# Optimization experiments

Measured on AMD Instinct MI355X. Metric: run time of the kernel, lower is better.

## Reference

```python
import jax, jax.numpy as jnp
import numpy as np

K = 32768          # random Fourier features of the integrand
MAX_DEPTH = 4      # fixed unroll depth of the adaptive quadtree


def _f_eval(px, py, w, ax, ay, phi):
    # integrand f(x,y) = sum_k w_k * cos(ax_k x + ay_k y + phi_k)
    theta = px[..., None] * ax + py[..., None] * ay + phi  # (..., K)
    return jnp.cos(theta) @ w


def _simpson_cells(xl, xr, yl, yr, w, ax, ay, phi):
    # 2D Simpson estimate per cell; matches _quad_simpsons2D_mem (center point
    # fp[4] has coefficient 0 in the original formula, so it is skipped).
    mx = (xl + xr) * 0.5
    my = (yl + yr) * 0.5
    px = jnp.stack([xl, mx, xr, xl, xr, xl, mx, xr], axis=-1)  # (N, 8)
    py = jnp.stack([yl, yl, yl, my, my, yr, yr, yr], axis=-1)
    fv = _f_eval(px, py, w, ax, ay, phi)                        # (N, 8)
    hx = jnp.abs(xr - xl)
    hy = jnp.abs(yr - yl)
    return hx * hy / 12.0 * (
        -(fv[..., 0] + fv[..., 2] + fv[..., 5] + fv[..., 7])
        + 4.0 * (fv[..., 1] + fv[..., 3] + fv[..., 4] + fv[..., 6]))


def _split(xl, xr, yl, yr):
    # children in quadrant order q0 (LL), q1 (LR), q2 (UL), q3 (UR), interleaved
    mx = (xl + xr) * 0.5
    my = (yl + yr) * 0.5
    cxl = jnp.stack([xl, mx, xl, mx], -1).reshape(-1)
    cxr = jnp.stack([mx, xr, mx, xr], -1).reshape(-1)
    cyl = jnp.stack([yl, yl, my, my], -1).reshape(-1)
    cyr = jnp.stack([my, my, yr, yr], -1).reshape(-1)
    return cxl, cxr, cyl, cyr


def _adaptive_simpson2d(xa, xb, ya, yb, eps, w, ax, ay, phi):
    xl = jnp.reshape(xa, (1,)); xr = jnp.reshape(xb, (1,))
    yl = jnp.reshape(ya, (1,)); yr = jnp.reshape(yb, (1,))
    bounds = [(xl, xr, yl, yr)]
    S = [_simpson_cells(xl, xr, yl, yr, w, ax, ay, phi)]  # (4**d,) per depth
    wholes = [S[0]]  # 'whole' passed into the asr call for each cell
    for d in range(1, MAX_DEPTH + 1):
        b = _split(*bounds[d - 1])
        bounds.append(b)
        Sd = _simpson_cells(*b, w, ax, ay, phi)
        S.append(Sd)
        W = Sd.reshape(-1, 4)
        # NOTE: original code passes q0 (not q3) as 'whole' for quadrant 3 --
        # this bug is reproduced faithfully.
        wholes.append(jnp.stack([W[:, 0], W[:, 1], W[:, 2], W[:, 0]], -1).reshape(-1))
    val = None
    for d in range(MAX_DEPTH - 1, -1, -1):
        sum_q = S[d + 1].reshape(-1, 4).sum(-1)
        delta = sum_q - wholes[d]
        corrected = sum_q + delta / 15.0
        if d == MAX_DEPTH - 1:
            val = corrected  # truncate recursion at max depth
        else:
            child_sum = val.reshape(-1, 4).sum(-1)
            eps_d = eps / (4.0 ** d)  # eps is quartered at each recursion level
            val = jnp.where(jnp.abs(delta) <= 15.0 * eps_d, corrected, child_sum)
    return val[0]


def setup_inputs() -> dict:
    key = jax.random.key(0)
    k1, k2, k3, k4 = jax.random.split(key, 4)
    w = jax.random.normal(k1, (K,), jnp.float32) / np.float32(np.sqrt(K))
    ax = jax.random.normal(k2, (K,), jnp.float32) * 6.0
    ay = jax.random.normal(k3, (K,), jnp.float32) * 6.0
    phi = jax.random.uniform(k4, (K,), jnp.float32) * np.float32(2.0 * np.pi)
    return {"xa": jnp.float32(0.0), "xb": jnp.float32(1.0),
            "ya": jnp.float32(0.0), "yb": jnp.float32(1.0),
            "eps": jnp.float32(1e-6),
            "w": w, "ax": ax, "ay": ay, "phi": phi}


def reference(xa, xb, ya, yb, eps, w, ax, ay, phi):
    return _adaptive_simpson2d(xa, xb, ya, yb, eps, w, ax, ay, phi)
```

## Files before the change

kernel.cpp:

```cpp
#include <hip/hip_runtime.h>
#include <math.h>

#define KFEAT 32768
#define GRID_N 33
#define NPTS (GRID_N * GRID_N)
#define NQ 833
#define QSTRIDE 836
#define QGROUPS (QSTRIDE / 4)
#define PTS_PER_BLOCK 8
#define PBLOCKS ((NQ + PTS_PER_BLOCK - 1) / PTS_PER_BLOCK)
#define SPLITK 8
#define KG 4

#define INV2PI 0.15915494309189535f

__device__ __forceinline__ void q_to_grid(int q, int& gx, int& gy) {
  int rp = q / 50;
  int rem = q - 50 * rp;
  if (rem < 33) { gy = 2 * rp;     gx = rem; }
  else          { gy = 2 * rp + 1; gx = (rem - 33) * 2; }
}

__device__ __forceinline__ float cos_rev(float rev) {
  float fr, c;
  asm("v_fract_f32 %0, %1" : "=v"(fr) : "v"(rev));
  asm("v_cos_f32 %0, %1" : "=v"(c) : "v"(fr));
  return c;
}

__global__ __launch_bounds__(256) void eval_grid_kernel(
    const float4* __restrict__ w4, const float4* __restrict__ ax4,
    const float4* __restrict__ ay4, const float4* __restrict__ phi4,
    const float* __restrict__ xa_p, const float* __restrict__ xb_p,
    const float* __restrict__ ya_p, const float* __restrict__ yb_p,
    float* __restrict__ Fpart) {
  const int tid = threadIdx.x;
  const int pblk = blockIdx.x;
  const int split = blockIdx.y;
  const float xa = xa_p[0], xb = xb_p[0];
  const float ya = ya_p[0], yb = yb_p[0];
  const float sx = (xb - xa) * (1.0f / 32.0f);
  const float sy = (yb - ya) * (1.0f / 32.0f);

  const int p0 = pblk * PTS_PER_BLOCK;
  float x[PTS_PER_BLOCK], y[PTS_PER_BLOCK];
#pragma unroll
  for (int j = 0; j < PTS_PER_BLOCK; ++j) {
    int q = min(p0 + j, NQ - 1);
    int gx, gy;
    q_to_grid(q, gx, gy);
    x[j] = fmaf((float)gx, sx, xa);
    y[j] = fmaf((float)gy, sy, ya);
  }

  const int base4 = split * ((KFEAT / 4) / SPLITK);
  float4 A[KG], B[KG], P[KG], W[KG];
#pragma unroll
  for (int u = 0; u < KG; ++u) {
    const int idx = base4 + tid + 256 * u;
    A[u] = ax4[idx];
    B[u] = ay4[idx];
    P[u] = phi4[idx];
    W[u] = w4[idx];
  }
#pragma unroll
  for (int u = 0; u < KG; ++u) {
    A[u].x *= INV2PI; A[u].y *= INV2PI; A[u].z *= INV2PI; A[u].w *= INV2PI;
    B[u].x *= INV2PI; B[u].y *= INV2PI; B[u].z *= INV2PI; B[u].w *= INV2PI;
    P[u].x *= INV2PI; P[u].y *= INV2PI; P[u].z *= INV2PI; P[u].w *= INV2PI;
  }

  float acc[PTS_PER_BLOCK];
#pragma unroll
  for (int j = 0; j < PTS_PER_BLOCK; ++j) acc[j] = 0.0f;

#pragma unroll
  for (int u = 0; u < KG; ++u) {
#pragma unroll
    for (int j = 0; j < PTS_PER_BLOCK; ++j) {
      float r0 = fmaf(A[u].x, x[j], fmaf(B[u].x, y[j], P[u].x));
      float r1 = fmaf(A[u].y, x[j], fmaf(B[u].y, y[j], P[u].y));
      float r2 = fmaf(A[u].z, x[j], fmaf(B[u].z, y[j], P[u].z));
      float r3 = fmaf(A[u].w, x[j], fmaf(B[u].w, y[j], P[u].w));
      float s = fmaf(W[u].x, cos_rev(r0), fmaf(W[u].y, cos_rev(r1),
                fmaf(W[u].z, cos_rev(r2), W[u].w * cos_rev(r3))));
      acc[j] += s;
    }
  }

  __shared__ float red[4][PTS_PER_BLOCK];
#pragma unroll
  for (int j = 0; j < PTS_PER_BLOCK; ++j) {
    float v = acc[j];
#pragma unroll
    for (int off = 32; off > 0; off >>= 1) v += __shfl_down(v, off, 64);
    if ((tid & 63) == 0) red[tid >> 6][j] = v;
  }
  __syncthreads();
  if (tid < PTS_PER_BLOCK) {
    const int j = tid;
    float v = red[0][j] + red[1][j] + red[2][j] + red[3][j];
    int q = p0 + j;
    if (q < NQ) Fpart[split * QSTRIDE + q] = v;
  }
}

__device__ __forceinline__ int compact_bits(int v, int shift) {
  int r = (v >> shift) & 1;
  r |= ((v >> (shift + 2)) & 1) << 1;
  r |= ((v >> (shift + 4)) & 1) << 2;
  r |= ((v >> (shift + 6)) & 1) << 3;
  return r;
}

__device__ __forceinline__ float simpson_cell(const float* __restrict__ F,
                                              int d, int cell, float hx,
                                              float hy) {
  const int ix = compact_bits(cell, 0);
  const int iy = compact_bits(cell, 1);
  const int s = 5 - d;
  const int h = 1 << (s - 1);
  const int gx0 = ix << s, gx1 = gx0 + h, gx2 = gx0 + 2 * h;
  const int gy0 = iy << s, gy1 = gy0 + h, gy2 = gy0 + 2 * h;
  const float f0 = F[gy0 * GRID_N + gx0];
  const float f1 = F[gy0 * GRID_N + gx1];
  const float f2 = F[gy0 * GRID_N + gx2];
  const float f3 = F[gy1 * GRID_N + gx0];
  const float f4 = F[gy1 * GRID_N + gx2];
  const float f5 = F[gy2 * GRID_N + gx0];
  const float f6 = F[gy2 * GRID_N + gx1];
  const float f7 = F[gy2 * GRID_N + gx2];
  return hx * hy * (1.0f / 12.0f) *
         (-(f0 + f2 + f5 + f7) + 4.0f * (f1 + f3 + f4 + f6));
}

__global__ __launch_bounds__(1024) void combine_kernel(
    const float* __restrict__ Fpart, const float* __restrict__ xa_p,
    const float* __restrict__ xb_p, const float* __restrict__ ya_p,
    const float* __restrict__ yb_p, const float* __restrict__ eps_p,
    float* __restrict__ out) {
  __shared__ alignas(16) float Fq[2][QSTRIDE];
  __shared__ float Fs[NPTS];
  __shared__ float S4[256], S3[64], S2[16], S1[4], S0[1];
  __shared__ float val3[64], val2[16], val1[4];
  const int t = threadIdx.x;
  const float xa = *xa_p, xb = *xb_p, ya = *ya_p, yb = *yb_p, eps = *eps_p;
  const float HX = fabsf(xb - xa), HY = fabsf(yb - ya);

  if (t < 2 * QGROUPS) {
    const int quad = (t >= QGROUPS) ? 1 : 0;
    const int g = t - quad * QGROUPS;
    const float4* Fp4 = (const float4*)Fpart;
    float4 s = make_float4(0.0f, 0.0f, 0.0f, 0.0f);
#pragma unroll
    for (int sp = 0; sp < 4; ++sp) {
      float4 v = Fp4[(quad * 4 + sp) * QGROUPS + g];
      s.x += v.x; s.y += v.y; s.z += v.z; s.w += v.w;
    }
    ((float4*)&Fq[quad][0])[g] = s;
  }
  __syncthreads();

  if (t < NQ) {
    float v = Fq[0][t] + Fq[1][t];
    int gx, gy;
    int rp = t / 50;
    int rem = t - 50 * rp;
    if (rem < 33) { gy = 2 * rp;     gx = rem; }
    else          { gy = 2 * rp + 1; gx = (rem - 33) * 2; }
    Fs[gy * GRID_N + gx] = v;
  }
  __syncthreads();

  if (t < 256) {
    S4[t] = simpson_cell(Fs, 4, t, HX * 0.0625f, HY * 0.0625f);
    if (t < 64) {
      S3[t] = simpson_cell(Fs, 3, t, HX * 0.125f, HY * 0.125f);
    } else if (t < 80) {
      S2[t - 64] = simpson_cell(Fs, 2, t - 64, HX * 0.25f, HY * 0.25f);
    } else if (t < 84) {
      S1[t - 80] = simpson_cell(Fs, 1, t - 80, HX * 0.5f, HY * 0.5f);
    } else if (t == 84) {
      S0[0] = simpson_cell(Fs, 0, 0, HX, HY);
    }
  }
  __syncthreads();

  if (t < 64) {
    float sumq = ((S4[4 * t] + S4[4 * t + 1]) + S4[4 * t + 2]) + S4[4 * t + 3];
    float whole = ((t & 3) == 3) ? S3[t & ~3] : S3[t];
    float delta = sumq - whole;
    val3[t] = sumq + delta * (1.0f / 15.0f);
  }
  __syncthreads();

  if (t < 16) {
    float sumq = ((S3[4 * t] + S3[4 * t + 1]) + S3[4 * t + 2]) + S3[4 * t + 3];
    float whole = ((t & 3) == 3) ? S2[t & ~3] : S2[t];
    float delta = sumq - whole;
    float corrected = sumq + delta * (1.0f / 15.0f);
    float child =
        ((val3[4 * t] + val3[4 * t + 1]) + val3[4 * t + 2]) + val3[4 * t + 3];
    float eps_d = eps * (1.0f / 16.0f);
    val2[t] = (fabsf(delta) <= 15.0f * eps_d) ? corrected : child;
  }
  __syncthreads();

  if (t < 4) {
    float sumq = ((S2[4 * t] + S2[4 * t + 1]) + S2[4 * t + 2]) + S2[4 * t + 3];
    float whole = ((t & 3) == 3) ? S1[t & ~3] : S1[t];
    float delta = sumq - whole;
    float corrected = sumq + delta * (1.0f / 15.0f);
    float child =
        ((val2[4 * t] + val2[4 * t + 1]) + val2[4 * t + 2]) + val2[4 * t + 3];
    float eps_d = eps * 0.25f;
    val1[t] = (fabsf(delta) <= 15.0f * eps_d) ? corrected : child;
  }
  __syncthreads();

  if (t == 0) {
    float sumq = ((S1[0] + S1[1]) + S1[2]) + S1[3];
    float delta = sumq - S0[0];
    float corrected = sumq + delta * (1.0f / 15.0f);
    float child = ((val1[0] + val1[1]) + val1[2]) + val1[3];
    out[0] = (fabsf(delta) <= 15.0f * eps) ? corrected : child;
  }
}

extern "C" void kernel_launch(void* const* d_in, const int* in_sizes, int n_in,
                              void* d_out, int out_size, void* d_ws,
                              size_t ws_size, hipStream_t stream) {
  const float* xa = (const float*)d_in[0];
  const float* xb = (const float*)d_in[1];
  const float* ya = (const float*)d_in[2];
  const float* yb = (const float*)d_in[3];
  const float* eps = (const float*)d_in[4];
  const float4* w4 = (const float4*)d_in[5];
  const float4* ax4 = (const float4*)d_in[6];
  const float4* ay4 = (const float4*)d_in[7];
  const float4* phi4 = (const float4*)d_in[8];
  float* out = (float*)d_out;
  float* Fpart = (float*)d_ws;

  dim3 grid(PBLOCKS, SPLITK);
  eval_grid_kernel<<<grid, 256, 0, stream>>>(w4, ax4, ay4, phi4, xa, xb, ya,
                                             yb, Fpart);
  combine_kernel<<<1, 1024, 0, stream>>>(Fpart, xa, xb, ya, yb, eps, out);
}
```

Baseline: 17.35 us.

## Evaluate grid rows with Chebyshev cosine recurrence instead of per-point cos

Each block now handles one row pair of the grid and, per feature, computes cosines along a row with the three-term recurrence cos((n+1)b+a) = 2cos(b)cos(nb+a) - cos((n-1)b+a). Only a few hardware cos calls are needed per feature per row, replacing one transcendental per point. The split over K grows to 32 with fewer blocks along the points, and the combine kernel is changed to reduce 32 partials using 256 threads. The recurrence can accumulate rounding error over 33 steps, and 50 accumulators per thread raise register pressure.

```diff
diff --git a/kernel.cpp b/kernel.cpp
--- a/kernel.cpp
+++ b/kernel.cpp
@@ -7,19 +7,11 @@
 #define NQ 833
 #define QSTRIDE 836
 #define QGROUPS (QSTRIDE / 4)
-#define PTS_PER_BLOCK 8
-#define PBLOCKS ((NQ + PTS_PER_BLOCK - 1) / PTS_PER_BLOCK)
-#define SPLITK 8
-#define KG 4
+#define NRP 17
+#define SPLITK 32
+#define KPT 4
 
 #define INV2PI 0.15915494309189535f
-
-__device__ __forceinline__ void q_to_grid(int q, int& gx, int& gy) {
-  int rp = q / 50;
-  int rem = q - 50 * rp;
-  if (rem < 33) { gy = 2 * rp;     gx = rem; }
-  else          { gy = 2 * rp + 1; gx = (rem - 33) * 2; }
-}
 
 __device__ __forceinline__ float cos_rev(float rev) {
   float fr, c;
@@ -28,80 +20,86 @@
   return c;
 }
 
-__global__ __launch_bounds__(256) void eval_grid_kernel(
+__global__ __launch_bounds__(256) void eval_rows_kernel(
     const float4* __restrict__ w4, const float4* __restrict__ ax4,
     const float4* __restrict__ ay4, const float4* __restrict__ phi4,
     const float* __restrict__ xa_p, const float* __restrict__ xb_p,
     const float* __restrict__ ya_p, const float* __restrict__ yb_p,
     float* __restrict__ Fpart) {
   const int tid = threadIdx.x;
-  const int pblk = blockIdx.x;
+  const int rp = blockIdx.x;
   const int split = blockIdx.y;
   const float xa = xa_p[0], xb = xb_p[0];
   const float ya = ya_p[0], yb = yb_p[0];
   const float sx = (xb - xa) * (1.0f / 32.0f);
   const float sy = (yb - ya) * (1.0f / 32.0f);
-
-  const int p0 = pblk * PTS_PER_BLOCK;
-  float x[PTS_PER_BLOCK], y[PTS_PER_BLOCK];
-#pragma unroll
-  for (int j = 0; j < PTS_PER_BLOCK; ++j) {
-    int q = min(p0 + j, NQ - 1);
-    int gx, gy;
-    q_to_grid(q, gx, gy);
-    x[j] = fmaf((float)gx, sx, xa);
-    y[j] = fmaf((float)gy, sy, ya);
-  }
-
-  const int base4 = split * ((KFEAT / 4) / SPLITK);
-  float4 A[KG], B[KG], P[KG], W[KG];
-#pragma unroll
-  for (int u = 0; u < KG; ++u) {
-    const int idx = base4 + tid + 256 * u;
-    A[u] = ax4[idx];
-    B[u] = ay4[idx];
-    P[u] = phi4[idx];
-    W[u] = w4[idx];
-  }
-#pragma unroll
-  for (int u = 0; u < KG; ++u) {
-    A[u].x *= INV2PI; A[u].y *= INV2PI; A[u].z *= INV2PI; A[u].w *= INV2PI;
-    B[u].x *= INV2PI; B[u].y *= INV2PI; B[u].z *= INV2PI; B[u].w *= INV2PI;
-    P[u].x *= INV2PI; P[u].y *= INV2PI; P[u].z *= INV2PI; P[u].w *= INV2PI;
-  }
-
-  float acc[PTS_PER_BLOCK];
-#pragma unroll
-  for (int j = 0; j < PTS_PER_BLOCK; ++j) acc[j] = 0.0f;
-
-#pragma unroll
-  for (int u = 0; u < KG; ++u) {
-#pragma unroll
-    for (int j = 0; j < PTS_PER_BLOCK; ++j) {
-      float r0 = fmaf(A[u].x, x[j], fmaf(B[u].x, y[j], P[u].x));
-      float r1 = fmaf(A[u].y, x[j], fmaf(B[u].y, y[j], P[u].y));
-      float r2 = fmaf(A[u].z, x[j], fmaf(B[u].z, y[j], P[u].z));
-      float r3 = fmaf(A[u].w, x[j], fmaf(B[u].w, y[j], P[u].w));
-      float s = fmaf(W[u].x, cos_rev(r0), fmaf(W[u].y, cos_rev(r1),
-                fmaf(W[u].z, cos_rev(r2), W[u].w * cos_rev(r3))));
-      acc[j] += s;
+  const float ye = fmaf((float)(2 * rp), sy, ya);
+
+  const int idx = split * (KFEAT / 4 / SPLITK) + tid;
+  float4 A4 = ax4[idx], B4 = ay4[idx], P4 = phi4[idx], W4 = w4[idx];
+  const float Aa[4] = {A4.x * INV2PI, A4.y * INV2PI, A4.z * INV2PI,
+                       A4.w * INV2PI};
+  const float Ba[4] = {B4.x * INV2PI, B4.y * INV2PI, B4.z * INV2PI,
+                       B4.w * INV2PI};
+  const float Pa[4] = {P4.x * INV2PI, P4.y * INV2PI, P4.z * INV2PI,
+                       P4.w * INV2PI};
+  const float Wa[4] = {W4.x, W4.y, W4.z, W4.w};
+
+  float acc[50];
+#pragma unroll
+  for (int j = 0; j < 50; ++j) acc[j] = 0.0f;
+
+#pragma unroll
+  for (int kk = 0; kk < KPT; ++kk) {
+    const float Ar = Aa[kk], Br = Ba[kk], Pr = Pa[kk], W = Wa[kk];
+    const float dr = Ar * sx;
+    const float cb = cos_rev(dr);
+    const float twob = cb + cb;
+    const float base = fmaf(Ar, xa, fmaf(Br, ye, Pr));
+    {
+      float d0 = W * cos_rev(base);
+      float d1 = W * cos_rev(base + dr);
+      acc[0] += d0;
+      acc[1] += d1;
+#pragma unroll
+      for (int n = 2; n < 33; ++n) {
+        float dn = fmaf(twob, d1, -d0);
+        acc[n] += dn;
+        d0 = d1;
+        d1 = dn;
+      }
     }
-  }
-
-  __shared__ float red[4][PTS_PER_BLOCK];
-#pragma unroll
-  for (int j = 0; j < PTS_PER_BLOCK; ++j) {
+    if (rp < 16) {
+      const float c2b = fmaf(twob, cb, -1.0f);
+      const float two2 = c2b + c2b;
+      const float baseo = fmaf(Br, sy, base);
+      float e0 = W * cos_rev(baseo);
+      float e1 = W * cos_rev(baseo + dr + dr);
+      acc[33] += e0;
+      acc[34] += e1;
+#pragma unroll
+      for (int g = 2; g < 17; ++g) {
+        float en = fmaf(two2, e1, -e0);
+        acc[33 + g] += en;
+        e0 = e1;
+        e1 = en;
+      }
+    }
+  }
+
+  __shared__ float red[4][50];
+#pragma unroll
+  for (int j = 0; j < 50; ++j) {
     float v = acc[j];
 #pragma unroll
     for (int off = 32; off > 0; off >>= 1) v += __shfl_down(v, off, 64);
     if ((tid & 63) == 0) red[tid >> 6][j] = v;
   }
   __syncthreads();
-  if (tid < PTS_PER_BLOCK) {
-    const int j = tid;
-    float v = red[0][j] + red[1][j] + red[2][j] + red[3][j];
-    int q = p0 + j;
-    if (q < NQ) Fpart[split * QSTRIDE + q] = v;
+  const int npts = (rp < 16) ? 50 : 33;
+  if (tid < npts) {
+    float v = red[0][tid] + red[1][tid] + red[2][tid] + red[3][tid];
+    Fpart[split * QSTRIDE + rp * 50 + tid] = v;
   }
 }
 
@@ -134,12 +132,12 @@
          (-(f0 + f2 + f5 + f7) + 4.0f * (f1 + f3 + f4 + f6));
 }
 
-__global__ __launch_bounds__(1024) void combine_kernel(
+__global__ __launch_bounds__(256) void combine_kernel(
     const float* __restrict__ Fpart, const float* __restrict__ xa_p,
     const float* __restrict__ xb_p, const float* __restrict__ ya_p,
     const float* __restrict__ yb_p, const float* __restrict__ eps_p,
     float* __restrict__ out) {
-  __shared__ alignas(16) float Fq[2][QSTRIDE];
+  __shared__ alignas(16) float Fq[4][QSTRIDE];
   __shared__ float Fs[NPTS];
   __shared__ float S4[256], S3[64], S2[16], S1[4], S0[1];
   __shared__ float val3[64], val2[16], val1[4];
@@ -147,42 +145,40 @@
   const float xa = *xa_p, xb = *xb_p, ya = *ya_p, yb = *yb_p, eps = *eps_p;
   const float HX = fabsf(xb - xa), HY = fabsf(yb - ya);
 
-  if (t < 2 * QGROUPS) {
-    const int quad = (t >= QGROUPS) ? 1 : 0;
-    const int g = t - quad * QGROUPS;
-    const float4* Fp4 = (const float4*)Fpart;
+  const float4* Fp4 = (const float4*)Fpart;
+  for (int task = t; task < 4 * QGROUPS; task += 256) {
+    const int g = task >> 2;
+    const int quad = task & 3;
     float4 s = make_float4(0.0f, 0.0f, 0.0f, 0.0f);
 #pragma unroll
-    for (int sp = 0; sp < 4; ++sp) {
-      float4 v = Fp4[(quad * 4 + sp) * QGROUPS + g];
+    for (int sp = 0; sp < 8; ++sp) {
+      float4 v = Fp4[(quad * 8 + sp) * QGROUPS + g];
       s.x += v.x; s.y += v.y; s.z += v.z; s.w += v.w;
     }
     ((float4*)&Fq[quad][0])[g] = s;
   }
   __syncthreads();
 
-  if (t < NQ) {
-    float v = Fq[0][t] + Fq[1][t];
+  for (int q = t; q < NQ; q += 256) {
+    float v = (Fq[0][q] + Fq[1][q]) + (Fq[2][q] + Fq[3][q]);
+    int rp = q / 50;
+    int rem = q - 50 * rp;
     int gx, gy;
-    int rp = t / 50;
-    int rem = t - 50 * rp;
     if (rem < 33) { gy = 2 * rp;     gx = rem; }
     else          { gy = 2 * rp + 1; gx = (rem - 33) * 2; }
     Fs[gy * GRID_N + gx] = v;
   }
   __syncthreads();
 
-  if (t < 256) {
-    S4[t] = simpson_cell(Fs, 4, t, HX * 0.0625f, HY * 0.0625f);
-    if (t < 64) {
-      S3[t] = simpson_cell(Fs, 3, t, HX * 0.125f, HY * 0.125f);
-    } else if (t < 80) {
-      S2[t - 64] = simpson_cell(Fs, 2, t - 64, HX * 0.25f, HY * 0.25f);
-    } else if (t < 84) {
-      S1[t - 80] = simpson_cell(Fs, 1, t - 80, HX * 0.5f, HY * 0.5f);
-    } else if (t == 84) {
-      S0[0] = simpson_cell(Fs, 0, 0, HX, HY);
-    }
+  S4[t] = simpson_cell(Fs, 4, t, HX * 0.0625f, HY * 0.0625f);
+  if (t < 64) {
+    S3[t] = simpson_cell(Fs, 3, t, HX * 0.125f, HY * 0.125f);
+  } else if (t < 80) {
+    S2[t - 64] = simpson_cell(Fs, 2, t - 64, HX * 0.25f, HY * 0.25f);
+  } else if (t < 84) {
+    S1[t - 80] = simpson_cell(Fs, 1, t - 80, HX * 0.5f, HY * 0.5f);
+  } else if (t == 84) {
+    S0[0] = simpson_cell(Fs, 0, 0, HX, HY);
   }
   __syncthreads();
 
@@ -242,8 +238,8 @@
   float* out = (float*)d_out;
   float* Fpart = (float*)d_ws;
 
-  dim3 grid(PBLOCKS, SPLITK);
-  eval_grid_kernel<<<grid, 256, 0, stream>>>(w4, ax4, ay4, phi4, xa, xb, ya,
+  dim3 grid(NRP, SPLITK);
+  eval_rows_kernel<<<grid, 256, 0, stream>>>(w4, ax4, ay4, phi4, xa, xb, ya,
                                              yb, Fpart);
-  combine_kernel<<<1, 1024, 0, stream>>>(Fpart, xa, xb, ya, yb, eps, out);
-}
+  combine_kernel<<<1, 256, 0, stream>>>(Fpart, xa, xb, ya, yb, eps, out);
+}
```

Measured after the change: 24.11 us. 39.0% more time.

## Fuse eval and combine kernels via last-block atomic counter

Applied to the files above, without the earlier changes.

Merges the grid-evaluation and combine kernels into a single launch. Each block writes its partial sums and then increments a global counter, and the last block to arrive performs the split-K reduction and the Simpson tree. This removes one kernel launch and the gap between kernels, but adds a memset launch to reset the counter. The combine step now runs on 256 threads instead of 1024.

```diff
diff --git a/kernel.cpp b/kernel.cpp
--- a/kernel.cpp
+++ b/kernel.cpp
@@ -6,103 +6,27 @@
 #define NPTS (GRID_N * GRID_N)
 #define NQ 833
 #define QSTRIDE 836
-#define QGROUPS (QSTRIDE / 4)
 #define PTS_PER_BLOCK 8
 #define PBLOCKS ((NQ + PTS_PER_BLOCK - 1) / PTS_PER_BLOCK)
 #define SPLITK 8
+#define NBLOCKS (PBLOCKS * SPLITK)
 #define KG 4
+#define COUNTER_OFFSET 27648
 
 #define INV2PI 0.15915494309189535f
+
+__device__ __forceinline__ float cos_rev(float rev) {
+  float fr, c;
+  asm("v_fract_f32 %0, %1" : "=v"(fr) : "v"(rev));
+  asm("v_cos_f32 %0, %1" : "=v"(c) : "v"(fr));
+  return c;
+}
 
 __device__ __forceinline__ void q_to_grid(int q, int& gx, int& gy) {
   int rp = q / 50;
   int rem = q - 50 * rp;
   if (rem < 33) { gy = 2 * rp;     gx = rem; }
   else          { gy = 2 * rp + 1; gx = (rem - 33) * 2; }
-}
-
-__device__ __forceinline__ float cos_rev(float rev) {
-  float fr, c;
-  asm("v_fract_f32 %0, %1" : "=v"(fr) : "v"(rev));
-  asm("v_cos_f32 %0, %1" : "=v"(c) : "v"(fr));
-  return c;
-}
-
-__global__ __launch_bounds__(256) void eval_grid_kernel(
-    const float4* __restrict__ w4, const float4* __restrict__ ax4,
-    const float4* __restrict__ ay4, const float4* __restrict__ phi4,
-    const float* __restrict__ xa_p, const float* __restrict__ xb_p,
-    const float* __restrict__ ya_p, const float* __restrict__ yb_p,
-    float* __restrict__ Fpart) {
-  const int tid = threadIdx.x;
-  const int pblk = blockIdx.x;
-  const int split = blockIdx.y;
-  const float xa = xa_p[0], xb = xb_p[0];
-  const float ya = ya_p[0], yb = yb_p[0];
-  const float sx = (xb - xa) * (1.0f / 32.0f);
-  const float sy = (yb - ya) * (1.0f / 32.0f);
-
-  const int p0 = pblk * PTS_PER_BLOCK;
-  float x[PTS_PER_BLOCK], y[PTS_PER_BLOCK];
-#pragma unroll
-  for (int j = 0; j < PTS_PER_BLOCK; ++j) {
-    int q = min(p0 + j, NQ - 1);
-    int gx, gy;
-    q_to_grid(q, gx, gy);
-    x[j] = fmaf((float)gx, sx, xa);
-    y[j] = fmaf((float)gy, sy, ya);
-  }
-
-  const int base4 = split * ((KFEAT / 4) / SPLITK);
-  float4 A[KG], B[KG], P[KG], W[KG];
-#pragma unroll
-  for (int u = 0; u < KG; ++u) {
-    const int idx = base4 + tid + 256 * u;
-    A[u] = ax4[idx];
-    B[u] = ay4[idx];
-    P[u] = phi4[idx];
-    W[u] = w4[idx];
-  }
-#pragma unroll
-  for (int u = 0; u < KG; ++u) {
-    A[u].x *= INV2PI; A[u].y *= INV2PI; A[u].z *= INV2PI; A[u].w *= INV2PI;
-    B[u].x *= INV2PI; B[u].y *= INV2PI; B[u].z *= INV2PI; B[u].w *= INV2PI;
-    P[u].x *= INV2PI; P[u].y *= INV2PI; P[u].z *= INV2PI; P[u].w *= INV2PI;
-  }
-
-  float acc[PTS_PER_BLOCK];
-#pragma unroll
-  for (int j = 0; j < PTS_PER_BLOCK; ++j) acc[j] = 0.0f;
-
-#pragma unroll
-  for (int u = 0; u < KG; ++u) {
-#pragma unroll
-    for (int j = 0; j < PTS_PER_BLOCK; ++j) {
-      float r0 = fmaf(A[u].x, x[j], fmaf(B[u].x, y[j], P[u].x));
-      float r1 = fmaf(A[u].y, x[j], fmaf(B[u].y, y[j], P[u].y));
-      float r2 = fmaf(A[u].z, x[j], fmaf(B[u].z, y[j], P[u].z));
-      float r3 = fmaf(A[u].w, x[j], fmaf(B[u].w, y[j], P[u].w));
-      float s = fmaf(W[u].x, cos_rev(r0), fmaf(W[u].y, cos_rev(r1),
-                fmaf(W[u].z, cos_rev(r2), W[u].w * cos_rev(r3))));
-      acc[j] += s;
-    }
-  }
-
-  __shared__ float red[4][PTS_PER_BLOCK];
-#pragma unroll
-  for (int j = 0; j < PTS_PER_BLOCK; ++j) {
-    float v = acc[j];
-#pragma unroll
-    for (int off = 32; off > 0; off >>= 1) v += __shfl_down(v, off, 64);
-    if ((tid & 63) == 0) red[tid >> 6][j] = v;
-  }
-  __syncthreads();
-  if (tid < PTS_PER_BLOCK) {
-    const int j = tid;
-    float v = red[0][j] + red[1][j] + red[2][j] + red[3][j];
-    int q = p0 + j;
-    if (q < NQ) Fpart[split * QSTRIDE + q] = v;
-  }
 }
 
 __device__ __forceinline__ int compact_bits(int v, int shift) {
@@ -134,45 +58,132 @@
          (-(f0 + f2 + f5 + f7) + 4.0f * (f1 + f3 + f4 + f6));
 }
 
-__global__ __launch_bounds__(1024) void combine_kernel(
-    const float* __restrict__ Fpart, const float* __restrict__ xa_p,
-    const float* __restrict__ xb_p, const float* __restrict__ ya_p,
-    const float* __restrict__ yb_p, const float* __restrict__ eps_p,
-    float* __restrict__ out) {
-  __shared__ alignas(16) float Fq[2][QSTRIDE];
-  __shared__ float Fs[NPTS];
-  __shared__ float S4[256], S3[64], S2[16], S1[4], S0[1];
-  __shared__ float val3[64], val2[16], val1[4];
-  const int t = threadIdx.x;
-  const float xa = *xa_p, xb = *xb_p, ya = *ya_p, yb = *yb_p, eps = *eps_p;
-  const float HX = fabsf(xb - xa), HY = fabsf(yb - ya);
-
-  if (t < 2 * QGROUPS) {
-    const int quad = (t >= QGROUPS) ? 1 : 0;
-    const int g = t - quad * QGROUPS;
-    const float4* Fp4 = (const float4*)Fpart;
-    float4 s = make_float4(0.0f, 0.0f, 0.0f, 0.0f);
-#pragma unroll
-    for (int sp = 0; sp < 4; ++sp) {
-      float4 v = Fp4[(quad * 4 + sp) * QGROUPS + g];
-      s.x += v.x; s.y += v.y; s.z += v.z; s.w += v.w;
-    }
-    ((float4*)&Fq[quad][0])[g] = s;
+__global__ __launch_bounds__(256) void fused_kernel(
+    const float4* __restrict__ w4, const float4* __restrict__ ax4,
+    const float4* __restrict__ ay4, const float4* __restrict__ phi4,
+    const float* __restrict__ xa_p, const float* __restrict__ xb_p,
+    const float* __restrict__ ya_p, const float* __restrict__ yb_p,
+    const float* __restrict__ eps_p, float* __restrict__ Fpart,
+    int* __restrict__ counter, float* __restrict__ out) {
+  const int tid = threadIdx.x;
+  const int split = blockIdx.x & (SPLITK - 1);
+  const int pblk = blockIdx.x >> 3;
+  const float xa = xa_p[0], xb = xb_p[0];
+  const float ya = ya_p[0], yb = yb_p[0];
+  const float sx = (xb - xa) * (1.0f / 32.0f);
+  const float sy = (yb - ya) * (1.0f / 32.0f);
+
+  {
+    const int p0 = pblk * PTS_PER_BLOCK;
+    float x[PTS_PER_BLOCK], y[PTS_PER_BLOCK];
+#pragma unroll
+    for (int j = 0; j < PTS_PER_BLOCK; ++j) {
+      int q = min(p0 + j, NQ - 1);
+      int gx, gy;
+      q_to_grid(q, gx, gy);
+      x[j] = fmaf((float)gx, sx, xa);
+      y[j] = fmaf((float)gy, sy, ya);
+    }
+
+    const int base4 = split * ((KFEAT / 4) / SPLITK);
+    float4 A[KG], B[KG], P[KG], W[KG];
+#pragma unroll
+    for (int u = 0; u < KG; ++u) {
+      const int idx = base4 + tid + 256 * u;
+      A[u] = ax4[idx];
+      B[u] = ay4[idx];
+      P[u] = phi4[idx];
+      W[u] = w4[idx];
+    }
+#pragma unroll
+    for (int u = 0; u < KG; ++u) {
+      A[u].x *= INV2PI; A[u].y *= INV2PI; A[u].z *= INV2PI; A[u].w *= INV2PI;
+      B[u].x *= INV2PI; B[u].y *= INV2PI; B[u].z *= INV2PI; B[u].w *= INV2PI;
+      P[u].x *= INV2PI; P[u].y *= INV2PI; P[u].z *= INV2PI; P[u].w *= INV2PI;
+    }
+
+    float acc[PTS_PER_BLOCK];
+#pragma unroll
+    for (int j = 0; j < PTS_PER_BLOCK; ++j) acc[j] = 0.0f;
+
+#pragma unroll
+    for (int u = 0; u < KG; ++u) {
+#pragma unroll
+      for (int j = 0; j < PTS_PER_BLOCK; ++j) {
+        float r0 = fmaf(A[u].x, x[j], fmaf(B[u].x, y[j], P[u].x));
+        float r1 = fmaf(A[u].y, x[j], fmaf(B[u].y, y[j], P[u].y));
+        float r2 = fmaf(A[u].z, x[j], fmaf(B[u].z, y[j], P[u].z));
+        float r3 = fmaf(A[u].w, x[j], fmaf(B[u].w, y[j], P[u].w));
+        float s = fmaf(W[u].x, cos_rev(r0), fmaf(W[u].y, cos_rev(r1),
+                  fmaf(W[u].z, cos_rev(r2), W[u].w * cos_rev(r3))));
+        acc[j] += s;
+      }
+    }
+
+    __shared__ float red[4][PTS_PER_BLOCK];
+#pragma unroll
+    for (int j = 0; j < PTS_PER_BLOCK; ++j) {
+      float v = acc[j];
+#pragma unroll
+      for (int off = 32; off > 0; off >>= 1) v += __shfl_down(v, off, 64);
+      if ((tid & 63) == 0) red[tid >> 6][j] = v;
+    }
+    __syncthreads();
+    if (tid < PTS_PER_BLOCK) {
+      const int j = tid;
+      float v = red[0][j] + red[1][j] + red[2][j] + red[3][j];
+      int q = p0 + j;
+      if (q < NQ) {
+        __hip_atomic_store(&Fpart[split * QSTRIDE + q], v, __ATOMIC_RELAXED,
+                           __HIP_MEMORY_SCOPE_AGENT);
+      }
+    }
+  }
+
+  __shared__ int is_last;
+  if (tid == 0) {
+    asm volatile("s_waitcnt vmcnt(0)" ::: "memory");
+    int old = __hip_atomic_fetch_add(counter, 1, __ATOMIC_RELAXED,
+                                     __HIP_MEMORY_SCOPE_AGENT);
+    is_last = (old == NBLOCKS - 1) ? 1 : 0;
   }
   __syncthreads();
-
-  if (t < NQ) {
-    float v = Fq[0][t] + Fq[1][t];
-    int gx, gy;
-    int rp = t / 50;
-    int rem = t - 50 * rp;
-    if (rem < 33) { gy = 2 * rp;     gx = rem; }
-    else          { gy = 2 * rp + 1; gx = (rem - 33) * 2; }
-    Fs[gy * GRID_N + gx] = v;
-  }
-  __syncthreads();
-
-  if (t < 256) {
+  if (!is_last) return;
+
+  {
+    __shared__ float Fsum[QSTRIDE];
+    __shared__ float Fs[NPTS];
+    __shared__ float S4[256], S3[64], S2[16], S1[4], S0[1];
+    __shared__ float val3[64], val2[16], val1[4];
+    const int t = tid;
+    const float eps = *eps_p;
+    const float HX = fabsf(xb - xa), HY = fabsf(yb - ya);
+
+    const unsigned long long* Fp8 = (const unsigned long long*)Fpart;
+    for (int task = t; task < QSTRIDE / 2; task += 256) {
+      float s0 = 0.0f, s1 = 0.0f;
+#pragma unroll
+      for (int sp = 0; sp < SPLITK; ++sp) {
+        unsigned long long v = __hip_atomic_load(
+            &Fp8[sp * (QSTRIDE / 2) + task], __ATOMIC_RELAXED,
+            __HIP_MEMORY_SCOPE_AGENT);
+        union { unsigned long long u; float f[2]; } cv;
+        cv.u = v;
+        s0 += cv.f[0];
+        s1 += cv.f[1];
+      }
+      Fsum[2 * task] = s0;
+      Fsum[2 * task + 1] = s1;
+    }
+    __syncthreads();
+
+    for (int q = t; q < NQ; q += 256) {
+      int gx, gy;
+      q_to_grid(q, gx, gy);
+      Fs[gy * GRID_N + gx] = Fsum[q];
+    }
+    __syncthreads();
+
     S4[t] = simpson_cell(Fs, 4, t, HX * 0.0625f, HY * 0.0625f);
     if (t < 64) {
       S3[t] = simpson_cell(Fs, 3, t, HX * 0.125f, HY * 0.125f);
@@ -183,47 +194,50 @@
     } else if (t == 84) {
       S0[0] = simpson_cell(Fs, 0, 0, HX, HY);
     }
-  }
-  __syncthreads();
-
-  if (t < 64) {
-    float sumq = ((S4[4 * t] + S4[4 * t + 1]) + S4[4 * t + 2]) + S4[4 * t + 3];
-    float whole = ((t & 3) == 3) ? S3[t & ~3] : S3[t];
-    float delta = sumq - whole;
-    val3[t] = sumq + delta * (1.0f / 15.0f);
-  }
-  __syncthreads();
-
-  if (t < 16) {
-    float sumq = ((S3[4 * t] + S3[4 * t + 1]) + S3[4 * t + 2]) + S3[4 * t + 3];
-    float whole = ((t & 3) == 3) ? S2[t & ~3] : S2[t];
-    float delta = sumq - whole;
-    float corrected = sumq + delta * (1.0f / 15.0f);
-    float child =
-        ((val3[4 * t] + val3[4 * t + 1]) + val3[4 * t + 2]) + val3[4 * t + 3];
-    float eps_d = eps * (1.0f / 16.0f);
-    val2[t] = (fabsf(delta) <= 15.0f * eps_d) ? corrected : child;
-  }
-  __syncthreads();
-
-  if (t < 4) {
-    float sumq = ((S2[4 * t] + S2[4 * t + 1]) + S2[4 * t + 2]) + S2[4 * t + 3];
-    float whole = ((t & 3) == 3) ? S1[t & ~3] : S1[t];
-    float delta = sumq - whole;
-    float corrected = sumq + delta * (1.0f / 15.0f);
-    float child =
-        ((val2[4 * t] + val2[4 * t + 1]) + val2[4 * t + 2]) + val2[4 * t + 3];
-    float eps_d = eps * 0.25f;
-    val1[t] = (fabsf(delta) <= 15.0f * eps_d) ? corrected : child;
-  }
-  __syncthreads();
-
-  if (t == 0) {
-    float sumq = ((S1[0] + S1[1]) + S1[2]) + S1[3];
-    float delta = sumq - S0[0];
-    float corrected = sumq + delta * (1.0f / 15.0f);
-    float child = ((val1[0] + val1[1]) + val1[2]) + val1[3];
-    out[0] = (fabsf(delta) <= 15.0f * eps) ? corrected : child;
+    __syncthreads();
+
+    if (t < 64) {
+      float sumq =
+          ((S4[4 * t] + S4[4 * t + 1]) + S4[4 * t + 2]) + S4[4 * t + 3];
+      float whole = ((t & 3) == 3) ? S3[t & ~3] : S3[t];
+      float delta = sumq - whole;
+      val3[t] = sumq + delta * (1.0f / 15.0f);
+    }
+    __syncthreads();
+
+    if (t < 16) {
+      float sumq =
+          ((S3[4 * t] + S3[4 * t + 1]) + S3[4 * t + 2]) + S3[4 * t + 3];
+      float whole = ((t & 3) == 3) ? S2[t & ~3] : S2[t];
+      float delta = sumq - whole;
+      float corrected = sumq + delta * (1.0f / 15.0f);
+      float child =
+          ((val3[4 * t] + val3[4 * t + 1]) + val3[4 * t + 2]) + val3[4 * t + 3];
+      float eps_d = eps * (1.0f / 16.0f);
+      val2[t] = (fabsf(delta) <= 15.0f * eps_d) ? corrected : child;
+    }
+    __syncthreads();
+
+    if (t < 4) {
+      float sumq =
+          ((S2[4 * t] + S2[4 * t + 1]) + S2[4 * t + 2]) + S2[4 * t + 3];
+      float whole = ((t & 3) == 3) ? S1[t & ~3] : S1[t];
+      float delta = sumq - whole;
+      float corrected = sumq + delta * (1.0f / 15.0f);
+      float child =
+          ((val2[4 * t] + val2[4 * t + 1]) + val2[4 * t + 2]) + val2[4 * t + 3];
+      float eps_d = eps * 0.25f;
+      val1[t] = (fabsf(delta) <= 15.0f * eps_d) ? corrected : child;
+    }
+    __syncthreads();
+
+    if (t == 0) {
+      float sumq = ((S1[0] + S1[1]) + S1[2]) + S1[3];
+      float delta = sumq - S0[0];
+      float corrected = sumq + delta * (1.0f / 15.0f);
+      float child = ((val1[0] + val1[1]) + val1[2]) + val1[3];
+      out[0] = (fabsf(delta) <= 15.0f * eps) ? corrected : child;
+    }
   }
 }
 
@@ -241,9 +255,10 @@
   const float4* phi4 = (const float4*)d_in[8];
   float* out = (float*)d_out;
   float* Fpart = (float*)d_ws;
-
-  dim3 grid(PBLOCKS, SPLITK);
-  eval_grid_kernel<<<grid, 256, 0, stream>>>(w4, ax4, ay4, phi4, xa, xb, ya,
-                                             yb, Fpart);
-  combine_kernel<<<1, 1024, 0, stream>>>(Fpart, xa, xb, ya, yb, eps, out);
-}
+  int* counter = (int*)((char*)d_ws + COUNTER_OFFSET);
+
+  hipMemsetAsync(counter, 0, sizeof(int), stream);
+
+  fused_kernel<<<NBLOCKS, 256, 0, stream>>>(w4, ax4, ay4, phi4, xa, xb, ya,
+                                            yb, eps, Fpart, counter, out);
+}
```

Measured after the change: 28.76 us. 1.66x slower.
